# Optimization experiments

Measured on AMD Instinct MI355X. Metric: run time of the kernel, lower is better.

The kernel has to match this reference:

```python
import jax, jax.numpy as jnp
import numpy as np

DX = 0.01
DT = 0.5
MU_UP = 0.001

_lap = np.array([[0,0,-1/12,0,0],[0,0,4/3,0,0],[-1/12,4/3,-5,4/3,-1/12],[0,0,4/3,0,0],[0,0,-1/12,0,0]], dtype=np.float32)
_dx = np.array([[0,0,1/12,0,0],[0,0,-8/12,0,0],[0,0,0,0,0],[0,0,8/12,0,0],[0,0,-1/12,0,0]], dtype=np.float32)
K_LAP = jnp.asarray(_lap)[None, None] / (DX * DX)   # [1,1,5,5]
K_DX = jnp.asarray(_dx)[None, None] / DX             # derivative along H axis (torch res_dx)
K_DY = jnp.swapaxes(K_DX, 2, 3)                      # derivative along W axis (torch res_dy)


def _conv(x, k):
    # cross-correlation, VALID, NCHW -- matches torch Conv2d
    return jax.lax.conv_general_dilated(x, k, (1, 1), 'VALID',
                                        dimension_numbers=('NCHW', 'OIHW', 'NCHW'))


def _pad(h):
    # periodic padding of 2 on both spatial dims (torch.cat based circular pad)
    return jnp.pad(h, ((0, 0), (0, 0), (2, 2), (2, 2)), mode='wrap')


def _f_rhs(u, v, Re, UA, UB, VA, VB):
    up, vp = _pad(u), _pad(v)
    u_x, u_y = _conv(up, K_DX), _conv(up, K_DY)
    v_x, v_y = _conv(vp, K_DX), _conv(vp, K_DY)
    nu = MU_UP / Re
    f_u = nu * _conv(up, K_LAP) + UA * u * u_x + UB * v * u_y
    f_v = nu * _conv(vp, K_LAP) + VA * u * v_x + VB * v * v_y
    return f_u, f_v


def setup_inputs() -> dict:
    key = jax.random.key(0)
    k_h, k_re, k_ua, k_ub, k_va, k_vb = jax.random.split(key, 6)
    h = jax.random.normal(k_h, (8, 2, 1024, 1024), dtype=jnp.float32)
    Re = jax.random.uniform(k_re, (), jnp.float32, 0.5, 1.5)  # keep 1/Re well-conditioned
    UA = jax.random.uniform(k_ua, (), jnp.float32)
    UB = jax.random.uniform(k_ub, (), jnp.float32)
    VA = jax.random.uniform(k_va, (), jnp.float32)
    VB = jax.random.uniform(k_vb, (), jnp.float32)
    return {'h': h, 'Re': Re, 'UA': UA, 'UB': UB, 'VA': VA, 'VB': VB}


def reference(h, Re, UA, UB, VA, VB):
    u0 = h[:, 0:1]
    v0 = h[:, 1:2]
    k1u, k1v = _f_rhs(u0, v0, Re, UA, UB, VA, VB)
    k2u, k2v = _f_rhs(u0 + k1u * (DT / 2.0), v0 + k1v * (DT / 2.0), Re, UA, UB, VA, VB)
    k3u, k3v = _f_rhs(u0 + k2u * (DT / 2.0), v0 + k2v * (DT / 2.0), Re, UA, UB, VA, VB)
    k4u, k4v = _f_rhs(u0 + k3u * DT, v0 + k3v * DT, Re, UA, UB, VA, VB)
    u_next = u0 + DT * (k1u + 2 * k2u + 2 * k3u + k4u) / 6.0
    v_next = v0 + DT * (k1v + 2 * k2v + 2 * k3v + k4v) / 6.0
    return jnp.concatenate((u_next, v_next), axis=1)
```

## Files before the change

### kernel.cpp

```cpp
#include <hip/hip_runtime.h>


typedef float f4 __attribute__((ext_vector_type(4)));
typedef float f2 __attribute__((ext_vector_type(2)));

#define LCOLS 100
#define LROWS 80
#define NFLD  8192
#define NT    1024
#define NQ    2

#define GLOAD16(gp, lp) __builtin_amdgcn_global_load_lds(                      \
    (const __attribute__((address_space(1))) void*)(gp),                       \
    (__attribute__((address_space(3))) void*)(lp), 16, 0, 0)

__global__ __launch_bounds__(NT, 4)
void rk4_stencil(const float* __restrict__ h,
                 const float* __restrict__ sRe, const float* __restrict__ sUA,
                 const float* __restrict__ sUB, const float* __restrict__ sVA,
                 const float* __restrict__ sVB, float* __restrict__ out)
{
    __shared__ __align__(16) float tu[NFLD];
    __shared__ __align__(16) float tv[NFLD];

    const int tid = threadIdx.x;
    const int tc = blockIdx.x, tr = blockIdx.y, bb = blockIdx.z;

    const float Re = sRe[0], UA = sUA[0], UB = sUB[0], VA = sVA[0], VB = sVB[0];
    const float nu = 0.001f / Re;

    const float d1 = 800.f/12.f;
    const float d2 = 100.f/12.f;
    const float a1 = (4.f/3.f)*1.0e4f;
    const float a2 = -(1.f/12.f)*1.0e4f;
    const float a0 = -5.0e4f;

    const f4 z4 = {0.f, 0.f, 0.f, 0.f};

    const size_t plane = 1048576;
    const float* uin = h + (size_t)(bb*2) * plane;
    const float* vin = uin + plane;
    const int base_r = tr*64 - 8  + 1024;
    const int base_c = tc*64 - 16 + 1024;

    {
        const int wave = tid >> 6, lane = tid & 63;
#pragma unroll
        for (int it = 0; it < 4; ++it) {
            int c = wave + 16*it;
            int fld = (c >= 32);
            int cc  = c & 31;
            int idx = 256*cc + 4*lane;
            int row = idx / LCOLS;
            int col = idx - row*LCOLS;
            int gr = (base_r + row) & 1023;
            int gc = (base_c + col) & 1023;
            const float* gp = (fld ? vin : uin) + ((size_t)gr << 10) + gc;
            float* lp = (fld ? tv : tu) + 256*cc;
            GLOAD16(gp, lp);
        }
    }
    __syncthreads();

    int  lidx[NQ]; bool has[NQ]; int qrA[NQ], qcA[NQ];
    f4 ku[NQ], kv[NQ], au[NQ], av[NQ];
    f4 stu[NQ], stv[NQ];
#pragma unroll
    for (int j = 0; j < NQ; ++j) {
        int q = tid + NT*j;
        has[j] = (j == 0) || (q < 1600);
        int qr = q % 80, qc = q / 80 + 2;
        qrA[j] = qr; qcA[j] = qc;
        lidx[j] = qr*LCOLS + 4*qc;
        ku[j] = z4; kv[j] = z4; au[j] = z4; av[j] = z4;
        stu[j] = z4; stv[j] = z4;
    }

    const int rowlo[4] = {2, 4, 6, 8};
    const int rowhi[4] = {78, 76, 74, 72};
    const int qclo[4]  = {2, 3, 3, 4};
    const int qchi[4]  = {22, 21, 21, 20};
    const float csub_t[4] = {0.f, 0.25f, 0.25f, 0.5f};
    const float cadd_t[4] = {0.25f, 0.25f, 0.5f, 0.f};
    const float wgt_t[4]  = {1.f, 2.f, 2.f, 1.f};

    float* outu = out + (size_t)(bb*2) * plane;
    float* outv = outu + plane;

#pragma unroll
    for (int s = 0; s < 4; ++s) {
        const float wgt  = wgt_t[s];
        const float csub = csub_t[s];
        const float cadd = cadd_t[s];
        bool act[NQ];
#pragma unroll
        for (int j = 0; j < NQ; ++j) {
            act[j] = has[j] && qrA[j] >= rowlo[s] && qrA[j] < rowhi[s]
                            && qcA[j] >= qclo[s]  && qcA[j] < qchi[s];
            if (!act[j]) continue;
            const int l = lidx[j];
            f4 ucc, vcc;
            if (s == 0) { ucc = *(const f4*)(tu+l); vcc = *(const f4*)(tv+l); }
            else        { ucc = stu[j];             vcc = stv[j]; }
            f2 ul2 = *(const f2*)(tu+l-2);
            f2 ur2 = *(const f2*)(tu+l+4);
            f4 un1 = *(const f4*)(tu+l-LCOLS);
            f4 us1 = *(const f4*)(tu+l+LCOLS);
            f4 un2 = *(const f4*)(tu+l-2*LCOLS);
            f4 us2 = *(const f4*)(tu+l+2*LCOLS);
            f2 vl2 = *(const f2*)(tv+l-2);
            f2 vr2 = *(const f2*)(tv+l+4);
            f4 vn1 = *(const f4*)(tv+l-LCOLS);
            f4 vs1 = *(const f4*)(tv+l+LCOLS);
            f4 vn2 = *(const f4*)(tv+l-2*LCOLS);
            f4 vs2 = *(const f4*)(tv+l+2*LCOLS);
            float hu[8] = {ul2[0],ul2[1],ucc[0],ucc[1],ucc[2],ucc[3],ur2[0],ur2[1]};
            float hv[8] = {vl2[0],vl2[1],vcc[0],vcc[1],vcc[2],vcc[3],vr2[0],vr2[1]};
            f4 ou, ov;
#pragma unroll
            for (int k = 0; k < 4; ++k) {
                float u = hu[k+2], v = hv[k+2];
                float urow = d1*(us1[k]-un1[k]) + d2*(un2[k]-us2[k]);
                float vrow = d1*(vs1[k]-vn1[k]) + d2*(vn2[k]-vs2[k]);
                float ucol = d1*(hu[k+3]-hu[k+1]) + d2*(hu[k]-hu[k+4]);
                float vcol = d1*(hv[k+3]-hv[k+1]) + d2*(hv[k]-hv[k+4]);
                float ulap = a1*((un1[k]+us1[k])+(hu[k+1]+hu[k+3]))
                           + a2*((un2[k]+us2[k])+(hu[k]+hu[k+4])) + a0*u;
                float vlap = a1*((vn1[k]+vs1[k])+(hv[k+1]+hv[k+3]))
                           + a2*((vn2[k]+vs2[k])+(hv[k]+hv[k+4])) + a0*v;
                float fu = nu*ulap + UA*(u*urow) + UB*(v*ucol);
                float fv = nu*vlap + VA*(u*vrow) + VB*(v*vcol);
                float kuold = ku[j][k], kvold = kv[j][k];
                if (s == 3) {
                    ou[k] = (u - 0.5f*kuold) + (1.f/12.f)*(au[j][k] + fu);
                    ov[k] = (v - 0.5f*kvold) + (1.f/12.f)*(av[j][k] + fv);
                } else {
                    au[j][k] += wgt*fu;
                    av[j][k] += wgt*fv;
                    stu[j][k] = (u - csub*kuold) + cadd*fu;
                    stv[j][k] = (v - csub*kvold) + cadd*fv;
                    ku[j][k] = fu;
                    kv[j][k] = fv;
                }
            }
            if (s == 3) {
                int gr = tr*64 + qrA[j] - 8;
                int gc = tc*64 + 4*qcA[j] - 16;
                *(f4*)(outu + (size_t)gr*1024 + gc) = ou;
                *(f4*)(outv + (size_t)gr*1024 + gc) = ov;
            }
        }
        if (s < 3) {
            __syncthreads();
#pragma unroll
            for (int j = 0; j < NQ; ++j) {
                if (!act[j]) continue;
                *(f4*)(tu+lidx[j]) = stu[j];
                *(f4*)(tv+lidx[j]) = stv[j];
            }
            __syncthreads();
        }
    }
}

extern "C" void kernel_launch(void* const* d_in, const int* in_sizes, int n_in,
                              void* d_out, int out_size, void* d_ws, size_t ws_size,
                              hipStream_t stream) {
    const float* h   = (const float*)d_in[0];
    const float* sRe = (const float*)d_in[1];
    const float* sUA = (const float*)d_in[2];
    const float* sUB = (const float*)d_in[3];
    const float* sVA = (const float*)d_in[4];
    const float* sVB = (const float*)d_in[5];
    float* o = (float*)d_out;
    rk4_stencil<<<dim3(16,16,8), dim3(NT,1,1), 0, stream>>>(h, sRe, sUA, sUB, sVA, sVB, o);
}
```

Before: 216.0 us.

## Remap threads to interior quads plus an ordered halo ring list per stage

Replaces the column-major quad assignment, where each thread owned up to two quads and tested per-stage bounds, with a fixed mapping. Each thread now owns one interior output quad, arranged as 4x16 quads per wave, plus an optional halo-ring quad. The ring quads are ordered so that each later stage's active set is a prefix of thread ids. This removes per-stage bound checks and divergence, and packs active ring work into contiguous waves. It also changes which LDS addresses a wave touches, which may alter bank-conflict behaviour.

```diff
diff --git a/kernel.cpp b/kernel.cpp
--- a/kernel.cpp
+++ b/kernel.cpp
@@ -5,14 +5,72 @@
 typedef float f2 __attribute__((ext_vector_type(2)));
 
 #define LCOLS 100
-#define LROWS 80
 #define NFLD  8192
 #define NT    1024
-#define NQ    2
 
 #define GLOAD16(gp, lp) __builtin_amdgcn_global_load_lds(                      \
     (const __attribute__((address_space(1))) void*)(gp),                       \
     (__attribute__((address_space(3))) void*)(lp), 16, 0, 0)
+
+template<int S>
+__device__ __forceinline__ void quad_stage(
+    const float* tu, const float* tv, int l,
+    float nu, float UA, float UB, float VA, float VB,
+    f4& ku, f4& kv, f4& au, f4& av, f4& su, f4& sv, f4& ou, f4& ov)
+{
+    const float csub = (S==0) ? 0.f : ((S==3) ? 0.5f : 0.25f);
+    const float cadd = (S<=1) ? 0.25f : ((S==2) ? 0.5f : 0.f);
+    const float wgt  = (S==1 || S==2) ? 2.f : 1.f;
+    const float d1 = 800.f/12.f;
+    const float d2 = 100.f/12.f;
+    const float a1 = (4.f/3.f)*1.0e4f;
+    const float a2 = -(1.f/12.f)*1.0e4f;
+    const float a0 = -5.0e4f;
+
+    f4 ucc, vcc;
+    if (S == 0) { ucc = *(const f4*)(tu+l); vcc = *(const f4*)(tv+l); }
+    else        { ucc = su;                 vcc = sv; }
+    f2 ul2 = *(const f2*)(tu+l-2);
+    f2 ur2 = *(const f2*)(tu+l+4);
+    f4 un1 = *(const f4*)(tu+l-LCOLS);
+    f4 us1 = *(const f4*)(tu+l+LCOLS);
+    f4 un2 = *(const f4*)(tu+l-2*LCOLS);
+    f4 us2 = *(const f4*)(tu+l+2*LCOLS);
+    f2 vl2 = *(const f2*)(tv+l-2);
+    f2 vr2 = *(const f2*)(tv+l+4);
+    f4 vn1 = *(const f4*)(tv+l-LCOLS);
+    f4 vs1 = *(const f4*)(tv+l+LCOLS);
+    f4 vn2 = *(const f4*)(tv+l-2*LCOLS);
+    f4 vs2 = *(const f4*)(tv+l+2*LCOLS);
+    float hu[8] = {ul2[0],ul2[1],ucc[0],ucc[1],ucc[2],ucc[3],ur2[0],ur2[1]};
+    float hv[8] = {vl2[0],vl2[1],vcc[0],vcc[1],vcc[2],vcc[3],vr2[0],vr2[1]};
+#pragma unroll
+    for (int k = 0; k < 4; ++k) {
+        float u = hu[k+2], v = hv[k+2];
+        float urow = d1*(us1[k]-un1[k]) + d2*(un2[k]-us2[k]);
+        float vrow = d1*(vs1[k]-vn1[k]) + d2*(vn2[k]-vs2[k]);
+        float ucol = d1*(hu[k+3]-hu[k+1]) + d2*(hu[k]-hu[k+4]);
+        float vcol = d1*(hv[k+3]-hv[k+1]) + d2*(hv[k]-hv[k+4]);
+        float ulap = a1*((un1[k]+us1[k])+(hu[k+1]+hu[k+3]))
+                   + a2*((un2[k]+us2[k])+(hu[k]+hu[k+4])) + a0*u;
+        float vlap = a1*((vn1[k]+vs1[k])+(hv[k+1]+hv[k+3]))
+                   + a2*((vn2[k]+vs2[k])+(hv[k]+hv[k+4])) + a0*v;
+        float fu = nu*ulap + UA*(u*urow) + UB*(v*ucol);
+        float fv = nu*vlap + VA*(u*vrow) + VB*(v*vcol);
+        float kuold = ku[k], kvold = kv[k];
+        if (S == 3) {
+            ou[k] = (u - 0.5f*kuold) + (1.f/12.f)*(au[k] + fu);
+            ov[k] = (v - 0.5f*kvold) + (1.f/12.f)*(av[k] + fv);
+        } else {
+            au[k] += wgt*fu;
+            av[k] += wgt*fv;
+            su[k] = (u - csub*kuold) + cadd*fu;
+            sv[k] = (v - csub*kvold) + cadd*fv;
+            ku[k] = fu;
+            kv[k] = fv;
+        }
+    }
+}
 
 __global__ __launch_bounds__(NT, 4)
 void rk4_stencil(const float* __restrict__ h,
@@ -28,13 +86,6 @@
 
     const float Re = sRe[0], UA = sUA[0], UB = sUB[0], VA = sVA[0], VB = sVB[0];
     const float nu = 0.001f / Re;
-
-    const float d1 = 800.f/12.f;
-    const float d2 = 100.f/12.f;
-    const float a1 = (4.f/3.f)*1.0e4f;
-    const float a2 = -(1.f/12.f)*1.0e4f;
-    const float a0 = -5.0e4f;
-
     const f4 z4 = {0.f, 0.f, 0.f, 0.f};
 
     const size_t plane = 1048576;
@@ -62,104 +113,64 @@
     }
     __syncthreads();
 
-    int  lidx[NQ]; bool has[NQ]; int qrA[NQ], qcA[NQ];
-    f4 ku[NQ], kv[NQ], au[NQ], av[NQ];
-    f4 stu[NQ], stv[NQ];
-#pragma unroll
-    for (int j = 0; j < NQ; ++j) {
-        int q = tid + NT*j;
-        has[j] = (j == 0) || (q < 1600);
-        int qr = q % 80, qc = q / 80 + 2;
-        qrA[j] = qr; qcA[j] = qc;
-        lidx[j] = qr*LCOLS + 4*qc;
-        ku[j] = z4; kv[j] = z4; au[j] = z4; av[j] = z4;
-        stu[j] = z4; stv[j] = z4;
+    const int wv = tid >> 6, ln = tid & 63;
+    const int dqr = 8 + 4*wv + (ln >> 4);
+    const int dqc = 4 + (ln & 15);
+    const int dl  = dqr*LCOLS + 4*dqc;
+
+    int rqr = 0, rqc = 0;
+    if (tid < 496) {
+        int i = tid;
+        if      (i < 36)  { rqr = 6  + i/18;       rqc = 3 + i%18; }
+        else if (i < 72)  { int t=i-36;  rqr = 72 + t/18; rqc = 3 + t%18; }
+        else if (i < 136) { rqr = 8 + (i-72);      rqc = 3; }
+        else if (i < 200) { rqr = 8 + (i-136);     rqc = 20; }
+        else if (i < 236) { int t=i-200; rqr = 4  + t/18; rqc = 3 + t%18; }
+        else if (i < 272) { int t=i-236; rqr = 74 + t/18; rqc = 3 + t%18; }
+        else if (i < 312) { int t=i-272; rqr = 2  + t/20; rqc = 2 + t%20; }
+        else if (i < 352) { int t=i-312; rqr = 76 + t/20; rqc = 2 + t%20; }
+        else if (i < 424) { rqr = 4 + (i-352);     rqc = 2; }
+        else              { rqr = 4 + (i-424);     rqc = 21; }
     }
+    const int rl = rqr*LCOLS + 4*rqc;
 
-    const int rowlo[4] = {2, 4, 6, 8};
-    const int rowhi[4] = {78, 76, 74, 72};
-    const int qclo[4]  = {2, 3, 3, 4};
-    const int qchi[4]  = {22, 21, 21, 20};
-    const float csub_t[4] = {0.f, 0.25f, 0.25f, 0.5f};
-    const float cadd_t[4] = {0.25f, 0.25f, 0.5f, 0.f};
-    const float wgt_t[4]  = {1.f, 2.f, 2.f, 1.f};
+    f4 dku=z4, dkv=z4, dau=z4, dav=z4, dsu=z4, dsv=z4;
+    f4 rku=z4, rkv=z4, rau=z4, rav=z4, rsu=z4, rsv=z4;
+    f4 du0=z4, du1=z4;
 
-    float* outu = out + (size_t)(bb*2) * plane;
-    float* outv = outu + plane;
+    quad_stage<0>(tu,tv,dl, nu,UA,UB,VA,VB, dku,dkv,dau,dav,dsu,dsv, du0,du1);
+    if (tid < 496)
+        quad_stage<0>(tu,tv,rl, nu,UA,UB,VA,VB, rku,rkv,rau,rav,rsu,rsv, du0,du1);
+    __syncthreads();
+    *(f4*)(tu+dl) = dsu; *(f4*)(tv+dl) = dsv;
+    if (tid < 496) { *(f4*)(tu+rl) = rsu; *(f4*)(tv+rl) = rsv; }
+    __syncthreads();
 
-#pragma unroll
-    for (int s = 0; s < 4; ++s) {
-        const float wgt  = wgt_t[s];
-        const float csub = csub_t[s];
-        const float cadd = cadd_t[s];
-        bool act[NQ];
-#pragma unroll
-        for (int j = 0; j < NQ; ++j) {
-            act[j] = has[j] && qrA[j] >= rowlo[s] && qrA[j] < rowhi[s]
-                            && qcA[j] >= qclo[s]  && qcA[j] < qchi[s];
-            if (!act[j]) continue;
-            const int l = lidx[j];
-            f4 ucc, vcc;
-            if (s == 0) { ucc = *(const f4*)(tu+l); vcc = *(const f4*)(tv+l); }
-            else        { ucc = stu[j];             vcc = stv[j]; }
-            f2 ul2 = *(const f2*)(tu+l-2);
-            f2 ur2 = *(const f2*)(tu+l+4);
-            f4 un1 = *(const f4*)(tu+l-LCOLS);
-            f4 us1 = *(const f4*)(tu+l+LCOLS);
-            f4 un2 = *(const f4*)(tu+l-2*LCOLS);
-            f4 us2 = *(const f4*)(tu+l+2*LCOLS);
-            f2 vl2 = *(const f2*)(tv+l-2);
-            f2 vr2 = *(const f2*)(tv+l+4);
-            f4 vn1 = *(const f4*)(tv+l-LCOLS);
-            f4 vs1 = *(const f4*)(tv+l+LCOLS);
-            f4 vn2 = *(const f4*)(tv+l-2*LCOLS);
-            f4 vs2 = *(const f4*)(tv+l+2*LCOLS);
-            float hu[8] = {ul2[0],ul2[1],ucc[0],ucc[1],ucc[2],ucc[3],ur2[0],ur2[1]};
-            float hv[8] = {vl2[0],vl2[1],vcc[0],vcc[1],vcc[2],vcc[3],vr2[0],vr2[1]};
-            f4 ou, ov;
-#pragma unroll
-            for (int k = 0; k < 4; ++k) {
-                float u = hu[k+2], v = hv[k+2];
-                float urow = d1*(us1[k]-un1[k]) + d2*(un2[k]-us2[k]);
-                float vrow = d1*(vs1[k]-vn1[k]) + d2*(vn2[k]-vs2[k]);
-                float ucol = d1*(hu[k+3]-hu[k+1]) + d2*(hu[k]-hu[k+4]);
-                float vcol = d1*(hv[k+3]-hv[k+1]) + d2*(hv[k]-hv[k+4]);
-                float ulap = a1*((un1[k]+us1[k])+(hu[k+1]+hu[k+3]))
-                           + a2*((un2[k]+us2[k])+(hu[k]+hu[k+4])) + a0*u;
-                float vlap = a1*((vn1[k]+vs1[k])+(hv[k+1]+hv[k+3]))
-                           + a2*((vn2[k]+vs2[k])+(hv[k]+hv[k+4])) + a0*v;
-                float fu = nu*ulap + UA*(u*urow) + UB*(v*ucol);
-                float fv = nu*vlap + VA*(u*vrow) + VB*(v*vcol);
-                float kuold = ku[j][k], kvold = kv[j][k];
-                if (s == 3) {
-                    ou[k] = (u - 0.5f*kuold) + (1.f/12.f)*(au[j][k] + fu);
-                    ov[k] = (v - 0.5f*kvold) + (1.f/12.f)*(av[j][k] + fv);
-                } else {
-                    au[j][k] += wgt*fu;
-                    av[j][k] += wgt*fv;
-                    stu[j][k] = (u - csub*kuold) + cadd*fu;
-                    stv[j][k] = (v - csub*kvold) + cadd*fv;
-                    ku[j][k] = fu;
-                    kv[j][k] = fv;
-                }
-            }
-            if (s == 3) {
-                int gr = tr*64 + qrA[j] - 8;
-                int gc = tc*64 + 4*qcA[j] - 16;
-                *(f4*)(outu + (size_t)gr*1024 + gc) = ou;
-                *(f4*)(outv + (size_t)gr*1024 + gc) = ov;
-            }
-        }
-        if (s < 3) {
-            __syncthreads();
-#pragma unroll
-            for (int j = 0; j < NQ; ++j) {
-                if (!act[j]) continue;
-                *(f4*)(tu+lidx[j]) = stu[j];
-                *(f4*)(tv+lidx[j]) = stv[j];
-            }
-            __syncthreads();
-        }
+    quad_stage<1>(tu,tv,dl, nu,UA,UB,VA,VB, dku,dkv,dau,dav,dsu,dsv, du0,du1);
+    if (tid < 272)
+        quad_stage<1>(tu,tv,rl, nu,UA,UB,VA,VB, rku,rkv,rau,rav,rsu,rsv, du0,du1);
+    __syncthreads();
+    *(f4*)(tu+dl) = dsu; *(f4*)(tv+dl) = dsv;
+    if (tid < 272) { *(f4*)(tu+rl) = rsu; *(f4*)(tv+rl) = rsv; }
+    __syncthreads();
+
+    quad_stage<2>(tu,tv,dl, nu,UA,UB,VA,VB, dku,dkv,dau,dav,dsu,dsv, du0,du1);
+    if (tid < 200)
+        quad_stage<2>(tu,tv,rl, nu,UA,UB,VA,VB, rku,rkv,rau,rav,rsu,rsv, du0,du1);
+    __syncthreads();
+    *(f4*)(tu+dl) = dsu; *(f4*)(tv+dl) = dsv;
+    if (tid < 200) { *(f4*)(tu+rl) = rsu; *(f4*)(tv+rl) = rsv; }
+    __syncthreads();
+
+    {
+        float* outu = out + (size_t)(bb*2) * plane;
+        float* outv = outu + plane;
+        f4 ou, ov;
+        quad_stage<3>(tu,tv,dl, nu,UA,UB,VA,VB, dku,dkv,dau,dav,dsu,dsv, ou,ov);
+        int gr = tr*64 + (dqr - 8);
+        int gc = tc*64 + 4*dqc - 16;
+        *(f4*)(outu + (size_t)gr*1024 + gc) = ou;
+        *(f4*)(outv + (size_t)gr*1024 + gc) = ov;
     }
 }
 
```

Result: no change. 211.9 us (-1.9%).

## Make stencil kernel persistent with double-buffered LDS tile prefetch

Applied to the files above, without the earlier changes.

Launches a fixed grid of 512 blocks that each loop over four tiles, staging the next tile into a second LDS buffer via async global-to-LDS loads while computing the current one. This aims to hide global load latency behind the RK4 stencil compute and cut block launch overhead. It doubles LDS per block to 128KB, which likely reduces resident blocks per CU and thus occupancy.

```diff
diff --git a/kernel.cpp b/kernel.cpp
--- a/kernel.cpp
+++ b/kernel.cpp
@@ -5,10 +5,11 @@
 typedef float f2 __attribute__((ext_vector_type(2)));
 
 #define LCOLS 100
-#define LROWS 80
 #define NFLD  8192
 #define NT    1024
 #define NQ    2
+#define NBLK  512
+#define TPB   4
 
 #define GLOAD16(gp, lp) __builtin_amdgcn_global_load_lds(                      \
     (const __attribute__((address_space(1))) void*)(gp),                       \
@@ -20,11 +21,10 @@
                  const float* __restrict__ sUB, const float* __restrict__ sVA,
                  const float* __restrict__ sVB, float* __restrict__ out)
 {
-    __shared__ __align__(16) float tu[NFLD];
-    __shared__ __align__(16) float tv[NFLD];
+    extern __shared__ __align__(16) float lds[];
 
     const int tid = threadIdx.x;
-    const int tc = blockIdx.x, tr = blockIdx.y, bb = blockIdx.z;
+    const int bx  = blockIdx.x;
 
     const float Re = sRe[0], UA = sUA[0], UB = sUB[0], VA = sVA[0], VB = sVB[0];
     const float nu = 0.001f / Re;
@@ -36,14 +36,16 @@
     const float a0 = -5.0e4f;
 
     const f4 z4 = {0.f, 0.f, 0.f, 0.f};
-
     const size_t plane = 1048576;
-    const float* uin = h + (size_t)(bb*2) * plane;
-    const float* vin = uin + plane;
-    const int base_r = tr*64 - 8  + 1024;
-    const int base_c = tc*64 - 16 + 1024;
-
-    {
+
+    auto stage_tile = [&](int t, int buf) {
+        const int tc = t & 15, tr = (t >> 4) & 15, bb = t >> 8;
+        const float* uin = h + (size_t)(bb*2) * plane;
+        const float* vin = uin + plane;
+        const int base_r = tr*64 - 8  + 1024;
+        const int base_c = tc*64 - 16 + 1024;
+        float* tub = lds + (buf ? 2*NFLD : 0);
+        float* tvb = tub + NFLD;
         const int wave = tid >> 6, lane = tid & 63;
 #pragma unroll
         for (int it = 0; it < 4; ++it) {
@@ -56,15 +58,12 @@
             int gr = (base_r + row) & 1023;
             int gc = (base_c + col) & 1023;
             const float* gp = (fld ? vin : uin) + ((size_t)gr << 10) + gc;
-            float* lp = (fld ? tv : tu) + 256*cc;
+            float* lp = (fld ? tvb : tub) + 256*cc;
             GLOAD16(gp, lp);
         }
-    }
-    __syncthreads();
+    };
 
     int  lidx[NQ]; bool has[NQ]; int qrA[NQ], qcA[NQ];
-    f4 ku[NQ], kv[NQ], au[NQ], av[NQ];
-    f4 stu[NQ], stv[NQ];
 #pragma unroll
     for (int j = 0; j < NQ; ++j) {
         int q = tid + NT*j;
@@ -72,8 +71,6 @@
         int qr = q % 80, qc = q / 80 + 2;
         qrA[j] = qr; qcA[j] = qc;
         lidx[j] = qr*LCOLS + 4*qc;
-        ku[j] = z4; kv[j] = z4; au[j] = z4; av[j] = z4;
-        stu[j] = z4; stv[j] = z4;
     }
 
     const int rowlo[4] = {2, 4, 6, 8};
@@ -84,82 +81,107 @@
     const float cadd_t[4] = {0.25f, 0.25f, 0.5f, 0.f};
     const float wgt_t[4]  = {1.f, 2.f, 2.f, 1.f};
 
-    float* outu = out + (size_t)(bb*2) * plane;
-    float* outv = outu + plane;
-
-#pragma unroll
-    for (int s = 0; s < 4; ++s) {
-        const float wgt  = wgt_t[s];
-        const float csub = csub_t[s];
-        const float cadd = cadd_t[s];
-        bool act[NQ];
+    stage_tile(bx, 0);
+    int cur = 0;
+
+#pragma unroll 1
+    for (int i = 0; i < TPB; ++i) {
+        const int t  = bx + i*NBLK;
+        const int tc = t & 15, tr = (t >> 4) & 15, bb = t >> 8;
+        float* tu = lds + (cur ? 2*NFLD : 0);
+        float* tv = tu + NFLD;
+
+        asm volatile("s_waitcnt vmcnt(0)" ::: "memory");
+        __syncthreads();
+
+        if (i + 1 < TPB) stage_tile(bx + (i+1)*NBLK, cur ^ 1);
+
+        f4 ku[NQ], kv[NQ], au[NQ], av[NQ];
+        f4 stu[NQ], stv[NQ];
 #pragma unroll
         for (int j = 0; j < NQ; ++j) {
-            act[j] = has[j] && qrA[j] >= rowlo[s] && qrA[j] < rowhi[s]
-                            && qcA[j] >= qclo[s]  && qcA[j] < qchi[s];
-            if (!act[j]) continue;
-            const int l = lidx[j];
-            f4 ucc, vcc;
-            if (s == 0) { ucc = *(const f4*)(tu+l); vcc = *(const f4*)(tv+l); }
-            else        { ucc = stu[j];             vcc = stv[j]; }
-            f2 ul2 = *(const f2*)(tu+l-2);
-            f2 ur2 = *(const f2*)(tu+l+4);
-            f4 un1 = *(const f4*)(tu+l-LCOLS);
-            f4 us1 = *(const f4*)(tu+l+LCOLS);
-            f4 un2 = *(const f4*)(tu+l-2*LCOLS);
-            f4 us2 = *(const f4*)(tu+l+2*LCOLS);
-            f2 vl2 = *(const f2*)(tv+l-2);
-            f2 vr2 = *(const f2*)(tv+l+4);
-            f4 vn1 = *(const f4*)(tv+l-LCOLS);
-            f4 vs1 = *(const f4*)(tv+l+LCOLS);
-            f4 vn2 = *(const f4*)(tv+l-2*LCOLS);
-            f4 vs2 = *(const f4*)(tv+l+2*LCOLS);
-            float hu[8] = {ul2[0],ul2[1],ucc[0],ucc[1],ucc[2],ucc[3],ur2[0],ur2[1]};
-            float hv[8] = {vl2[0],vl2[1],vcc[0],vcc[1],vcc[2],vcc[3],vr2[0],vr2[1]};
-            f4 ou, ov;
-#pragma unroll
-            for (int k = 0; k < 4; ++k) {
-                float u = hu[k+2], v = hv[k+2];
-                float urow = d1*(us1[k]-un1[k]) + d2*(un2[k]-us2[k]);
-                float vrow = d1*(vs1[k]-vn1[k]) + d2*(vn2[k]-vs2[k]);
-                float ucol = d1*(hu[k+3]-hu[k+1]) + d2*(hu[k]-hu[k+4]);
-                float vcol = d1*(hv[k+3]-hv[k+1]) + d2*(hv[k]-hv[k+4]);
-                float ulap = a1*((un1[k]+us1[k])+(hu[k+1]+hu[k+3]))
-                           + a2*((un2[k]+us2[k])+(hu[k]+hu[k+4])) + a0*u;
-                float vlap = a1*((vn1[k]+vs1[k])+(hv[k+1]+hv[k+3]))
-                           + a2*((vn2[k]+vs2[k])+(hv[k]+hv[k+4])) + a0*v;
-                float fu = nu*ulap + UA*(u*urow) + UB*(v*ucol);
-                float fv = nu*vlap + VA*(u*vrow) + VB*(v*vcol);
-                float kuold = ku[j][k], kvold = kv[j][k];
+            ku[j] = z4; kv[j] = z4; au[j] = z4; av[j] = z4;
+            stu[j] = z4; stv[j] = z4;
+        }
+
+        float* outu = out + (size_t)(bb*2) * plane;
+        float* outv = outu + plane;
+
+#pragma unroll
+        for (int s = 0; s < 4; ++s) {
+            const float wgt  = wgt_t[s];
+            const float csub = csub_t[s];
+            const float cadd = cadd_t[s];
+            bool act[NQ];
+#pragma unroll
+            for (int j = 0; j < NQ; ++j) {
+                act[j] = has[j] && qrA[j] >= rowlo[s] && qrA[j] < rowhi[s]
+                                && qcA[j] >= qclo[s]  && qcA[j] < qchi[s];
+                if (!act[j]) continue;
+                const int l = lidx[j];
+                f4 ucc, vcc;
+                if (s == 0) { ucc = *(const f4*)(tu+l); vcc = *(const f4*)(tv+l); }
+                else        { ucc = stu[j];             vcc = stv[j]; }
+                f2 ul2 = *(const f2*)(tu+l-2);
+                f2 ur2 = *(const f2*)(tu+l+4);
+                f4 un1 = *(const f4*)(tu+l-LCOLS);
+                f4 us1 = *(const f4*)(tu+l+LCOLS);
+                f4 un2 = *(const f4*)(tu+l-2*LCOLS);
+                f4 us2 = *(const f4*)(tu+l+2*LCOLS);
+                f2 vl2 = *(const f2*)(tv+l-2);
+                f2 vr2 = *(const f2*)(tv+l+4);
+                f4 vn1 = *(const f4*)(tv+l-LCOLS);
+                f4 vs1 = *(const f4*)(tv+l+LCOLS);
+                f4 vn2 = *(const f4*)(tv+l-2*LCOLS);
+                f4 vs2 = *(const f4*)(tv+l+2*LCOLS);
+                float hu[8] = {ul2[0],ul2[1],ucc[0],ucc[1],ucc[2],ucc[3],ur2[0],ur2[1]};
+                float hv[8] = {vl2[0],vl2[1],vcc[0],vcc[1],vcc[2],vcc[3],vr2[0],vr2[1]};
+                f4 ou, ov;
+#pragma unroll
+                for (int k = 0; k < 4; ++k) {
+                    float u = hu[k+2], v = hv[k+2];
+                    float urow = d1*(us1[k]-un1[k]) + d2*(un2[k]-us2[k]);
+                    float vrow = d1*(vs1[k]-vn1[k]) + d2*(vn2[k]-vs2[k]);
+                    float ucol = d1*(hu[k+3]-hu[k+1]) + d2*(hu[k]-hu[k+4]);
+                    float vcol = d1*(hv[k+3]-hv[k+1]) + d2*(hv[k]-hv[k+4]);
+                    float ulap = a1*((un1[k]+us1[k])+(hu[k+1]+hu[k+3]))
+                               + a2*((un2[k]+us2[k])+(hu[k]+hu[k+4])) + a0*u;
+                    float vlap = a1*((vn1[k]+vs1[k])+(hv[k+1]+hv[k+3]))
+                               + a2*((vn2[k]+vs2[k])+(hv[k]+hv[k+4])) + a0*v;
+                    float fu = nu*ulap + UA*(u*urow) + UB*(v*ucol);
+                    float fv = nu*vlap + VA*(u*vrow) + VB*(v*vcol);
+                    float kuold = ku[j][k], kvold = kv[j][k];
+                    if (s == 3) {
+                        ou[k] = (u - 0.5f*kuold) + (1.f/12.f)*(au[j][k] + fu);
+                        ov[k] = (v - 0.5f*kvold) + (1.f/12.f)*(av[j][k] + fv);
+                    } else {
+                        au[j][k] += wgt*fu;
+                        av[j][k] += wgt*fv;
+                        stu[j][k] = (u - csub*kuold) + cadd*fu;
+                        stv[j][k] = (v - csub*kvold) + cadd*fv;
+                        ku[j][k] = fu;
+                        kv[j][k] = fv;
+                    }
+                }
                 if (s == 3) {
-                    ou[k] = (u - 0.5f*kuold) + (1.f/12.f)*(au[j][k] + fu);
-                    ov[k] = (v - 0.5f*kvold) + (1.f/12.f)*(av[j][k] + fv);
-                } else {
-                    au[j][k] += wgt*fu;
-                    av[j][k] += wgt*fv;
-                    stu[j][k] = (u - csub*kuold) + cadd*fu;
-                    stv[j][k] = (v - csub*kvold) + cadd*fv;
-                    ku[j][k] = fu;
-                    kv[j][k] = fv;
+                    int gr = tr*64 + qrA[j] - 8;
+                    int gc = tc*64 + 4*qcA[j] - 16;
+                    *(f4*)(outu + (size_t)gr*1024 + gc) = ou;
+                    *(f4*)(outv + (size_t)gr*1024 + gc) = ov;
                 }
             }
-            if (s == 3) {
-                int gr = tr*64 + qrA[j] - 8;
-                int gc = tc*64 + 4*qcA[j] - 16;
-                *(f4*)(outu + (size_t)gr*1024 + gc) = ou;
-                *(f4*)(outv + (size_t)gr*1024 + gc) = ov;
+            if (s < 3) {
+                __syncthreads();
+#pragma unroll
+                for (int j = 0; j < NQ; ++j) {
+                    if (!act[j]) continue;
+                    *(f4*)(tu+lidx[j]) = stu[j];
+                    *(f4*)(tv+lidx[j]) = stv[j];
+                }
+                __syncthreads();
             }
         }
-        if (s < 3) {
-            __syncthreads();
-#pragma unroll
-            for (int j = 0; j < NQ; ++j) {
-                if (!act[j]) continue;
-                *(f4*)(tu+lidx[j]) = stu[j];
-                *(f4*)(tv+lidx[j]) = stv[j];
-            }
-            __syncthreads();
-        }
+        cur ^= 1;
     }
 }
 
@@ -173,5 +195,14 @@
     const float* sVA = (const float*)d_in[4];
     const float* sVB = (const float*)d_in[5];
     float* o = (float*)d_out;
-    rk4_stencil<<<dim3(16,16,8), dim3(NT,1,1), 0, stream>>>(h, sRe, sUA, sUB, sVA, sVB, o);
+
+    static bool s_attr = false;
+    if (!s_attr) {
+        hipFuncSetAttribute((const void*)rk4_stencil,
+                            hipFuncAttributeMaxDynamicSharedMemorySize,
+                            4 * NFLD * (int)sizeof(float));
+        s_attr = true;
+    }
+    rk4_stencil<<<dim3(NBLK,1,1), dim3(NT,1,1), 4*NFLD*sizeof(float), stream>>>(
+        h, sRe, sUA, sUB, sVA, sVB, o);
 }
```

Result: faster. 207.7 us (-3.9%).
